# Kernel optimization log

Measured on AMD Instinct MI355X. Metric: run time of the kernel, lower is better.

## Reference

```python
import jax, jax.numpy as jnp
import numpy as np

GH, GW = 7, 7            # hierarchical grid size
LN_EPS = 1e-5            # torch nn.LayerNorm default eps
NEG = -1e9


def _adaptive_avg_pool2d(x, oh, ow):
    # Replicates torch F.adaptive_avg_pool2d bin boundaries:
    # start=floor(i*H/out), end=ceil((i+1)*H/out). x: (..., H, W)
    H, W = x.shape[-2], x.shape[-1]
    def b(i, n, o):
        return int(np.floor(i * n / o)), int(np.ceil((i + 1) * n / o))
    rows = jnp.stack([x[..., b(i, H, oh)[0]:b(i, H, oh)[1], :].mean(axis=-2)
                      for i in range(oh)], axis=-2)
    out = jnp.stack([rows[..., b(j, W, ow)[0]:b(j, W, ow)[1]].mean(axis=-1)
                     for j in range(ow)], axis=-1)
    return out


def _layernorm(y, gamma, beta):
    mu = y.mean(axis=-1, keepdims=True)
    var = jnp.mean(jnp.square(y - mu), axis=-1, keepdims=True)
    return (y - mu) * jax.lax.rsqrt(var + LN_EPS) * gamma + beta


def setup_inputs() -> dict:
    key = jax.random.key(0)
    ks = jax.random.split(key, 16)
    B, C, H, W = 8, 512, 32, 32
    heads = 8
    s = 0.02
    f32 = jnp.float32
    return {
        "x":    jax.random.normal(ks[0], (B, C, H, W), f32),
        "Wq":   jax.random.normal(ks[1], (C, C), f32) * s,
        "bq":   jnp.zeros((C,), f32),
        "Wk":   jax.random.normal(ks[2], (C, C), f32) * s,
        "bk":   jnp.zeros((C,), f32),
        "Wv":   jax.random.normal(ks[3], (C, C), f32) * s,
        "bv":   jnp.zeros((C,), f32),
        "Wo":   jax.random.normal(ks[4], (C, C), f32) * s,
        "bo":   jnp.zeros((C,), f32),
        "Wsp":  jax.random.normal(ks[5], (heads, C), f32) * s,   # 1x1 conv C->heads
        "bsp":  jnp.zeros((heads,), f32),
        "Wse1": jax.random.normal(ks[6], (C // 16, C), f32) * s, # SE squeeze
        "bse1": jnp.zeros((C // 16,), f32),
        "Wse2": jax.random.normal(ks[7], (C, C // 16), f32) * s, # SE excite
        "bse2": jnp.zeros((C,), f32),
        "gamma": jnp.ones((C,), f32),
        "beta":  jnp.zeros((C,), f32),
    }


def reference(x, Wq, bq, Wk, bk, Wv, bv, Wo, bo, Wsp, bsp,
              Wse1, bse1, Wse2, bse2, gamma, beta):
    B, C, H, W = x.shape
    heads = Wsp.shape[0]
    d = C // heads
    N = H * W

    # --- hierarchical grid mask ---
    sp = jnp.einsum('bchw,nc->bnhw', x, Wsp) + bsp[None, :, None, None]
    m = jax.nn.sigmoid(sp)                               # (B, heads, H, W)
    mg = _adaptive_avg_pool2d(m, GH, GW)
    mg = (mg > 0.5).astype(x.dtype)                      # binarize
    ih = np.floor(np.arange(H) * GH / H).astype(np.int32)  # torch 'nearest'
    iw = np.floor(np.arange(W) * GW / W).astype(np.int32)
    mask = mg[..., ih[:, None], iw[None, :]]             # (B, heads, H, W)

    # --- SE channel gating ---
    pooled = x.mean(axis=(2, 3))                         # (B, C)
    h1 = jax.nn.relu(pooled @ Wse1.T + bse1)
    cw = jax.nn.sigmoid(h1 @ Wse2.T + bse2)              # (B, C)
    xf = (x * cw[:, :, None, None]).reshape(B, C, N).transpose(0, 2, 1)  # (B,N,C)

    # --- multi-head attention with outer-product additive mask ---
    def heads_split(t):
        return t.reshape(B, N, heads, d).transpose(0, 2, 1, 3)  # (B,h,N,d)
    Q = heads_split(xf @ Wq.T + bq)
    K = heads_split(xf @ Wk.T + bk)
    V = heads_split(xf @ Wv.T + bv)

    scores = jnp.einsum('bhnd,bhmd->bhnm', Q, K) / (d ** 0.5)
    mf = mask.reshape(B, heads, N)
    bias = (1.0 - mf[:, :, :, None] * mf[:, :, None, :]) * NEG
    w = jax.nn.softmax(scores + bias, axis=-1)
    attn = jnp.einsum('bhnm,bhmd->bhnd', w, V)
    attn = attn.transpose(0, 2, 1, 3).reshape(B, N, C)
    attn = attn @ Wo.T + bo

    y = _layernorm(xf + attn, gamma, beta)               # (B, N, C)
    return y.transpose(0, 2, 1).reshape(B, C, H, W)
```

## Files before the change

### kernel.cpp

```cpp
#include <hip/hip_runtime.h>
#include <hip/hip_bf16.h>
#include <math.h>

typedef unsigned short u16;
typedef unsigned int u32;
typedef __attribute__((ext_vector_type(4))) float f32x4;
typedef __attribute__((ext_vector_type(8))) short bf16x8;
typedef __attribute__((ext_vector_type(4))) unsigned short us4;
typedef __attribute__((ext_vector_type(8))) unsigned short us8;

#define DI __device__ __forceinline__

DI u16 f2b(float x){ __hip_bfloat16 h = __float2bfloat16(x); return *reinterpret_cast<u16*>(&h); }
DI float b2f(u16 u){ union { float f; u32 i; } v; v.i = ((u32)u) << 16; return v.f; }

__global__ void k_cvt(const float* __restrict__ Wq, const float* __restrict__ Wk,
                      const float* __restrict__ Wv, const float* __restrict__ Wo,
                      u16* __restrict__ WB, u16* __restrict__ WoB){
  int i = blockIdx.x * 256 + threadIdx.x;
  WB[i]          = f2b(Wq[i]);
  WB[262144 + i] = f2b(Wk[i]);
  WB[524288 + i] = f2b(Wv[i]);
  WoB[i]         = f2b(Wo[i]);
}

__global__ __launch_bounds__(256) void k_pooled(const float* __restrict__ x, float* __restrict__ pooled){
  int row  = blockIdx.x * 4 + (threadIdx.x >> 6);
  int lane = threadIdx.x & 63;
  const float4* p = (const float4*)(x + ((size_t)row << 10));
  float4 v0 = p[lane], v1 = p[lane + 64], v2 = p[lane + 128], v3 = p[lane + 192];
  float s = (v0.x + v0.y + v0.z + v0.w) + (v1.x + v1.y + v1.z + v1.w)
          + (v2.x + v2.y + v2.z + v2.w) + (v3.x + v3.y + v3.z + v3.w);
  #pragma unroll
  for (int o = 32; o > 0; o >>= 1) s += __shfl_down(s, o, 64);
  if (lane == 0) pooled[row] = s * (1.0f / 1024.0f);
}

__global__ __launch_bounds__(256) void k_se(const float* __restrict__ pooled,
    const float* __restrict__ Wse1, const float* __restrict__ bse1,
    const float* __restrict__ Wse2, const float* __restrict__ bse2,
    float* __restrict__ cw){
  __shared__ float pl[512];
  __shared__ float h1[32];
  int b = blockIdx.x, t = threadIdx.x;
  pl[t] = pooled[b * 512 + t];
  pl[t + 256] = pooled[b * 512 + t + 256];
  __syncthreads();
  if (t < 32){
    float acc = bse1[t];
    const float* w = Wse1 + t * 512;
    for (int c = 0; c < 512; c++) acc = fmaf(pl[c], w[c], acc);
    h1[t] = fmaxf(acc, 0.0f);
  }
  __syncthreads();
  for (int c = t; c < 512; c += 256){
    float acc = bse2[c];
    const float* w = Wse2 + c * 32;
    #pragma unroll
    for (int j = 0; j < 32; j++) acc = fmaf(h1[j], w[j], acc);
    cw[b * 512 + c] = 1.0f / (1.0f + expf(-acc));
  }
}

__global__ __launch_bounds__(256) void k_sp(const float* __restrict__ x,
    const float* __restrict__ Wsp, const float* __restrict__ bsp, float* __restrict__ mbuf){
  __shared__ float wsh[4096];
  __shared__ float part[4][512];
  int t = threadIdx.x;
  for (int i = t; i < 4096; i += 256) wsh[i] = Wsp[i];
  __syncthreads();
  int b = blockIdx.x >> 4, n0 = (blockIdx.x & 15) << 6;
  int px = t & 63, cq = t >> 6;
  const float* xp = x + ((size_t)b << 19) + ((size_t)(cq * 128) << 10) + n0 + px;
  float acc[8] = {0,0,0,0,0,0,0,0};
  for (int c = 0; c < 128; c++){
    float xv = xp[(size_t)c << 10];
    #pragma unroll
    for (int h = 0; h < 8; h++) acc[h] = fmaf(xv, wsh[(h << 9) + cq * 128 + c], acc[h]);
  }
  #pragma unroll
  for (int h = 0; h < 8; h++) part[cq][(h << 6) + px] = acc[h];
  __syncthreads();
  for (int i = t; i < 512; i += 256){
    int h = i >> 6, p = i & 63;
    float s = part[0][i] + part[1][i] + part[2][i] + part[3][i] + bsp[h];
    mbuf[(((size_t)(b * 8 + h)) << 10) + n0 + p] = 1.0f / (1.0f + expf(-s));
  }
}

__global__ void k_mask(const float* __restrict__ mbuf, float* __restrict__ bneg){
  __shared__ float sm[1024];
  __shared__ float mg[49];
  int bh = blockIdx.x, t = threadIdx.x;
  const float* mp = mbuf + ((size_t)bh << 10);
  for (int i = t; i < 1024; i += 64) sm[i] = mp[i];
  __syncthreads();
  if (t < 49){
    int ci = t / 7, cj = t % 7;
    int r0 = (ci * 32) / 7, r1 = ((ci + 1) * 32 + 6) / 7;
    int c0 = (cj * 32) / 7, c1 = ((cj + 1) * 32 + 6) / 7;
    float acc = 0.0f;
    for (int cc = c0; cc < c1; cc++){
      float rs = 0.0f;
      for (int rr = r0; rr < r1; rr++) rs += sm[rr * 32 + cc];
      acc += rs / (float)(r1 - r0);
    }
    float v = acc / (float)(c1 - c0);
    mg[t] = (v > 0.5f) ? 1.0f : 0.0f;
  }
  __syncthreads();
  for (int i = t; i < 1024; i += 64){
    int r = i >> 5, c = i & 31;
    float m = mg[((r * 7) >> 5) * 7 + ((c * 7) >> 5)];
    bneg[((size_t)bh << 10) + i] = (m > 0.5f) ? 0.0f : -1e9f;
  }
}

__global__ __launch_bounds__(256) void k_xf(const float* __restrict__ x,
    const float* __restrict__ cw, u16* __restrict__ xfB){
  __shared__ float tile[64][65];
  int bid = blockIdx.x;
  int b = bid >> 7, c0 = ((bid >> 4) & 7) << 6, n0 = (bid & 15) << 6;
  int t = threadIdx.x;
  {
    int cl = t >> 2, nc = (t & 3) << 4;
    const float* xp = x + ((size_t)(b * 512 + c0 + cl) << 10) + n0 + nc;
    float cwv = cw[b * 512 + c0 + cl];
    #pragma unroll
    for (int i = 0; i < 16; i += 4){
      float4 v = *(const float4*)(xp + i);
      tile[cl][nc + i + 0] = v.x * cwv;
      tile[cl][nc + i + 1] = v.y * cwv;
      tile[cl][nc + i + 2] = v.z * cwv;
      tile[cl][nc + i + 3] = v.w * cwv;
    }
  }
  __syncthreads();
  {
    int nl = t >> 2, cc = (t & 3) << 4;
    u16* op = xfB + ((size_t)(b * 1024 + n0 + nl) << 9) + c0 + cc;
    us8 o0, o1;
    #pragma unroll
    for (int i = 0; i < 8; i++)  o0[i] = f2b(tile[cc + i][nl]);
    #pragma unroll
    for (int i = 0; i < 8; i++)  o1[i] = f2b(tile[cc + 8 + i][nl]);
    *(us8*)op = o0;
    *(us8*)(op + 8) = o1;
  }
}

template<int MODE>
__global__ __launch_bounds__(256) void k_gemm(const u16* __restrict__ A, const u16* __restrict__ Bw,
    const float* __restrict__ b0, const float* __restrict__ b1, const float* __restrict__ b2,
    u16* __restrict__ outQ, u16* __restrict__ outK, u16* __restrict__ outV, float* __restrict__ outF){
  __shared__ u16 As[128 * 40];
  __shared__ u16 Bs[128 * 40];
  int m0 = blockIdx.x * 128, n0 = blockIdx.y * 128;
  int t = threadIdx.x, lane = t & 63, w = t >> 6;
  int wr = w >> 1, wc = w & 1;
  f32x4 acc[4][4];
  #pragma unroll
  for (int mt = 0; mt < 4; mt++)
    #pragma unroll
    for (int nt = 0; nt < 4; nt++) acc[mt][nt] = (f32x4){0.f, 0.f, 0.f, 0.f};

  int srow = t >> 1, scol = (t & 1) << 4;
  const u16* ap = A  + (size_t)(m0 + srow) * 512 + scol;
  const u16* bp = Bw + (size_t)(n0 + srow) * 512 + scol;

  for (int k0 = 0; k0 < 512; k0 += 32){
    uint4 av0 = *(const uint4*)(ap + k0);
    uint4 av1 = *(const uint4*)(ap + k0 + 8);
    uint4 bv0 = *(const uint4*)(bp + k0);
    uint4 bv1 = *(const uint4*)(bp + k0 + 8);
    *(uint4*)&As[srow * 40 + scol]     = av0;
    *(uint4*)&As[srow * 40 + scol + 8] = av1;
    *(uint4*)&Bs[srow * 40 + scol]     = bv0;
    *(uint4*)&Bs[srow * 40 + scol + 8] = bv1;
    __syncthreads();
    bf16x8 afr[4], bfr[4];
    #pragma unroll
    for (int mt = 0; mt < 4; mt++)
      afr[mt] = *(bf16x8*)&As[(wr * 64 + mt * 16 + (lane & 15)) * 40 + ((lane >> 4) << 3)];
    #pragma unroll
    for (int nt = 0; nt < 4; nt++)
      bfr[nt] = *(bf16x8*)&Bs[(wc * 64 + nt * 16 + (lane & 15)) * 40 + ((lane >> 4) << 3)];
    #pragma unroll
    for (int mt = 0; mt < 4; mt++)
      #pragma unroll
      for (int nt = 0; nt < 4; nt++)
        acc[mt][nt] = __builtin_amdgcn_mfma_f32_16x16x32_bf16(afr[mt], bfr[nt], acc[mt][nt], 0, 0, 0);
    __syncthreads();
  }

  #pragma unroll
  for (int mt = 0; mt < 4; mt++){
    #pragma unroll
    for (int nt = 0; nt < 4; nt++){
      int o = n0 + wc * 64 + nt * 16 + (lane & 15);
      int mb = m0 + wr * 64 + mt * 16 + ((lane >> 4) << 2);
      if (MODE == 0){
        int which = o >> 9, c = o & 511;
        int h = c >> 6, d = c & 63;
        int b = mb >> 10, n = mb & 1023;
        if (which == 2){
          float bias = b2[c];
          int nperm = (n & ~31) + (((n >> 2) & 3) << 3) + (((n >> 4) & 1) << 2);
          us4 pk;
          #pragma unroll
          for (int j = 0; j < 4; j++) pk[j] = f2b(acc[mt][nt][j] + bias);
          *(us4*)&outV[(((size_t)(b * 8 + h)) << 16) + ((size_t)d << 10) + nperm] = pk;
        } else {
          float bias = (which == 0) ? b0[c] : b1[c];
          u16* base = (which == 0) ? outQ : outK;
          #pragma unroll
          for (int j = 0; j < 4; j++)
            base[(((size_t)(b * 8 + h)) << 16) + ((size_t)(n + j) << 6) + d] = f2b(acc[mt][nt][j] + bias);
        }
      } else {
        float bias = b0[o];
        #pragma unroll
        for (int j = 0; j < 4; j++)
          outF[((size_t)(mb + j) << 9) + o] = acc[mt][nt][j] + bias;
      }
    }
  }
}

__global__ __launch_bounds__(256) void k_flash(const u16* __restrict__ Q, const u16* __restrict__ K,
    const u16* __restrict__ Vt, const float* __restrict__ bneg, u16* __restrict__ attnB){
  __shared__ u16 Ks[64 * 72];
  __shared__ u16 Vts[64 * 72];
  __shared__ float mks[64];
  int bid = blockIdx.x;
  int bh = bid >> 4, q0 = (bid & 15) << 6;
  int t = threadIdx.x, lane = t & 63, w = t >> 6;
  int g = lane >> 4, li = lane & 15;

  const u16* Kp = K  + ((size_t)bh << 16);
  const u16* Vp = Vt + ((size_t)bh << 16);
  const float* bp = bneg + ((size_t)bh << 10);

  bf16x8 qfr0, qfr1;
  {
    const u16* qrow = Q + ((size_t)bh << 16) + ((size_t)(q0 + w * 16 + li) << 6);
    qfr0 = *(const bf16x8*)(qrow + g * 8);
    qfr1 = *(const bf16x8*)(qrow + 32 + g * 8);
  }
  float bnq = bp[q0 + w * 16 + li];

  f32x4 oacc[4];
  #pragma unroll
  for (int dt = 0; dt < 4; dt++) oacc[dt] = (f32x4){0.f, 0.f, 0.f, 0.f};
  float mrun = -INFINITY, lrun = 0.0f;

  int sr = t >> 2, sc = (t & 3) << 4;
  const u16* kg = Kp + ((size_t)sr << 6) + sc;
  const u16* vg = Vp + ((size_t)sr << 10) + sc;
  uint4 kr0, kr1, vr0, vr1;
  float mr = 0.0f;
  kr0 = *(const uint4*)(kg);
  kr1 = *(const uint4*)(kg + 8);
  vr0 = *(const uint4*)(vg);
  vr1 = *(const uint4*)(vg + 8);
  if (t < 64) mr = bp[t];

  for (int kt = 0; kt < 16; kt++){
    __syncthreads();
    *(uint4*)&Ks[sr * 72 + sc]      = kr0;
    *(uint4*)&Ks[sr * 72 + sc + 8]  = kr1;
    *(uint4*)&Vts[sr * 72 + sc]     = vr0;
    *(uint4*)&Vts[sr * 72 + sc + 8] = vr1;
    if (t < 64) mks[t] = mr;
    if (kt < 15){
      kr0 = *(const uint4*)(kg + (kt + 1) * 4096);
      kr1 = *(const uint4*)(kg + (kt + 1) * 4096 + 8);
      vr0 = *(const uint4*)(vg + (kt + 1) * 64);
      vr1 = *(const uint4*)(vg + (kt + 1) * 64 + 8);
      if (t < 64) mr = bp[(kt + 1) * 64 + t];
    }
    __syncthreads();

    f32x4 sacc[4];
    #pragma unroll
    for (int mt = 0; mt < 4; mt++) sacc[mt] = (f32x4){0.f, 0.f, 0.f, 0.f};
    #pragma unroll
    for (int mt = 0; mt < 4; mt++){
      bf16x8 kfr0 = *(bf16x8*)&Ks[(mt * 16 + li) * 72 + g * 8];
      bf16x8 kfr1 = *(bf16x8*)&Ks[(mt * 16 + li) * 72 + 32 + g * 8];
      sacc[mt] = __builtin_amdgcn_mfma_f32_16x16x32_bf16(kfr0, qfr0, sacc[mt], 0, 0, 0);
      sacc[mt] = __builtin_amdgcn_mfma_f32_16x16x32_bf16(kfr1, qfr1, sacc[mt], 0, 0, 0);
    }

    float tmax = -INFINITY;
    #pragma unroll
    for (int mt = 0; mt < 4; mt++){
      float4 bk = *(const float4*)&mks[mt * 16 + g * 4];
      float bkk[4] = {bk.x, bk.y, bk.z, bk.w};
      #pragma unroll
      for (int j = 0; j < 4; j++){
        float s = sacc[mt][j] * 0.125f + fminf(bkk[j], bnq);
        sacc[mt][j] = s;
        tmax = fmaxf(tmax, s);
      }
    }
    tmax = fmaxf(tmax, __shfl_xor(tmax, 16, 64));
    tmax = fmaxf(tmax, __shfl_xor(tmax, 32, 64));
    float mnew = fmaxf(mrun, tmax);
    float scl = __expf(mrun - mnew);
    mrun = mnew;

    float rsum = 0.0f;
    #pragma unroll
    for (int mt = 0; mt < 4; mt++)
      #pragma unroll
      for (int j = 0; j < 4; j++){
        float p = __expf(sacc[mt][j] - mnew);
        sacc[mt][j] = p;
        rsum += p;
      }
    rsum += __shfl_xor(rsum, 16, 64);
    rsum += __shfl_xor(rsum, 32, 64);
    lrun = lrun * scl + rsum;
    #pragma unroll
    for (int dt = 0; dt < 4; dt++)
      #pragma unroll
      for (int j = 0; j < 4; j++) oacc[dt][j] *= scl;

    bf16x8 pfr0, pfr1;
    #pragma unroll
    for (int e = 0; e < 4; e++){
      pfr0[e]     = (short)f2b(sacc[0][e]);
      pfr0[4 + e] = (short)f2b(sacc[1][e]);
      pfr1[e]     = (short)f2b(sacc[2][e]);
      pfr1[4 + e] = (short)f2b(sacc[3][e]);
    }
    #pragma unroll
    for (int dt = 0; dt < 4; dt++){
      bf16x8 vfr0 = *(bf16x8*)&Vts[(dt * 16 + li) * 72 + g * 8];
      bf16x8 vfr1 = *(bf16x8*)&Vts[(dt * 16 + li) * 72 + 32 + g * 8];
      oacc[dt] = __builtin_amdgcn_mfma_f32_16x16x32_bf16(vfr0, pfr0, oacc[dt], 0, 0, 0);
      oacc[dt] = __builtin_amdgcn_mfma_f32_16x16x32_bf16(vfr1, pfr1, oacc[dt], 0, 0, 0);
    }
  }

  float inv = 1.0f / lrun;
  int b = bh >> 3, h = bh & 7;
  u16* op = attnB + (((size_t)(b * 1024 + q0 + w * 16 + li)) << 9) + h * 64 + g * 4;
  #pragma unroll
  for (int dt = 0; dt < 4; dt++){
    us4 pk;
    #pragma unroll
    for (int j = 0; j < 4; j++) pk[j] = f2b(oacc[dt][j] * inv);
    *(us4*)(op + dt * 16) = pk;
  }
}

__global__ __launch_bounds__(256) void k_ln(const u16* __restrict__ xfB, const float* __restrict__ attnO,
    const float* __restrict__ gamma, const float* __restrict__ beta, float* __restrict__ out){
  __shared__ float mu_s[64], rs_s[64];
  __shared__ float tile[64][65];
  int b = blockIdx.x >> 4, n0 = (blockIdx.x & 15) << 6;
  int t = threadIdx.x, w = t >> 6, lane = t & 63;

  for (int r = w * 16; r < w * 16 + 16; r++){
    size_t rb = ((size_t)(b * 1024 + n0 + r)) << 9;
    const float* ap = attnO + rb + lane * 8;
    const u16*  xp = xfB + rb + lane * 8;
    float4 a0 = *(const float4*)ap;
    float4 a1 = *(const float4*)(ap + 4);
    union { uint4 v; u16 u[8]; } xv; xv.v = *(const uint4*)xp;
    float v0 = a0.x + b2f(xv.u[0]), v1 = a0.y + b2f(xv.u[1]);
    float v2 = a0.z + b2f(xv.u[2]), v3 = a0.w + b2f(xv.u[3]);
    float v4 = a1.x + b2f(xv.u[4]), v5 = a1.y + b2f(xv.u[5]);
    float v6 = a1.z + b2f(xv.u[6]), v7 = a1.w + b2f(xv.u[7]);
    float s  = v0 + v1 + v2 + v3 + v4 + v5 + v6 + v7;
    float s2 = v0*v0 + v1*v1 + v2*v2 + v3*v3 + v4*v4 + v5*v5 + v6*v6 + v7*v7;
    #pragma unroll
    for (int o = 32; o > 0; o >>= 1){ s += __shfl_xor(s, o, 64); s2 += __shfl_xor(s2, o, 64); }
    if (lane == 0){
      float mu = s * (1.0f / 512.0f);
      float var = s2 * (1.0f / 512.0f) - mu * mu;
      mu_s[r] = mu;
      rs_s[r] = 1.0f / sqrtf(var + 1e-5f);
    }
  }
  __syncthreads();

  for (int ch = 0; ch < 8; ch++){
    int c0 = ch * 64;
    {
      int r = t >> 2, cp = (t & 3) << 4;
      size_t rb = (((size_t)(b * 1024 + n0 + r)) << 9) + c0 + cp;
      float mu = mu_s[r], rstd = rs_s[r];
      #pragma unroll
      for (int i2 = 0; i2 < 2; i2++){
        float4 a0 = *(const float4*)(attnO + rb + i2 * 8);
        float4 a1 = *(const float4*)(attnO + rb + i2 * 8 + 4);
        union { uint4 v; u16 u[8]; } xv; xv.v = *(const uint4*)(xfB + rb + i2 * 8);
        float vv[8] = { a0.x + b2f(xv.u[0]), a0.y + b2f(xv.u[1]), a0.z + b2f(xv.u[2]), a0.w + b2f(xv.u[3]),
                        a1.x + b2f(xv.u[4]), a1.y + b2f(xv.u[5]), a1.z + b2f(xv.u[6]), a1.w + b2f(xv.u[7]) };
        #pragma unroll
        for (int i = 0; i < 8; i++){
          int c = c0 + cp + i2 * 8 + i;
          tile[r][cp + i2 * 8 + i] = (vv[i] - mu) * rstd * gamma[c] + beta[c];
        }
      }
    }
    __syncthreads();
    {
      int cl = t >> 2, np_ = (t & 3) << 4;
      float* op = out + (((size_t)(b * 512 + c0 + cl)) << 10) + n0 + np_;
      #pragma unroll
      for (int i = 0; i < 16; i += 4){
        float4 vo = { tile[np_ + i][cl], tile[np_ + i + 1][cl], tile[np_ + i + 2][cl], tile[np_ + i + 3][cl] };
        *(float4*)(op + i) = vo;
      }
    }
    __syncthreads();
  }
}

extern "C" void kernel_launch(void* const* d_in, const int* in_sizes, int n_in,
                              void* d_out, int out_size, void* d_ws, size_t ws_size,
                              hipStream_t stream){
  (void)in_sizes; (void)n_in; (void)out_size; (void)ws_size;
  const float* x    = (const float*)d_in[0];
  const float* Wq   = (const float*)d_in[1];
  const float* bq   = (const float*)d_in[2];
  const float* Wk   = (const float*)d_in[3];
  const float* bk   = (const float*)d_in[4];
  const float* Wv   = (const float*)d_in[5];
  const float* bv   = (const float*)d_in[6];
  const float* Wo   = (const float*)d_in[7];
  const float* bo   = (const float*)d_in[8];
  const float* Wsp  = (const float*)d_in[9];
  const float* bsp  = (const float*)d_in[10];
  const float* Wse1 = (const float*)d_in[11];
  const float* bse1 = (const float*)d_in[12];
  const float* Wse2 = (const float*)d_in[13];
  const float* bse2 = (const float*)d_in[14];
  const float* gamma= (const float*)d_in[15];
  const float* beta = (const float*)d_in[16];
  float* out = (float*)d_out;

  char* ws = (char*)d_ws;
  size_t off = 0;
  auto alloc = [&](size_t bytes) -> void* {
    void* p = ws + off;
    off += (bytes + 255) & ~(size_t)255;
    return p;
  };
  u16*   WB     = (u16*)  alloc(1536 * 512 * 2);
  u16*   WoB    = (u16*)  alloc(512 * 512 * 2);
  float* pooled = (float*)alloc(4096 * 4);
  float* cw     = (float*)alloc(4096 * 4);
  float* mbuf   = (float*)alloc(65536 * 4);
  float* bneg   = (float*)alloc(65536 * 4);
  u16*   xfB    = (u16*)  alloc((size_t)8192 * 512 * 2);
  u16*   Qb     = (u16*)  alloc(8388608);
  u16*   Kb     = (u16*)  alloc(8388608);
  u16*   VtG    = (u16*)  alloc(8388608);
  u16*   attnB  = (u16*)  alloc(8388608);
  float* attnO  = (float*)Qb;

  k_cvt   <<<dim3(1024), dim3(256), 0, stream>>>(Wq, Wk, Wv, Wo, WB, WoB);
  k_pooled<<<dim3(1024), dim3(256), 0, stream>>>(x, pooled);
  k_se    <<<dim3(8),    dim3(256), 0, stream>>>(pooled, Wse1, bse1, Wse2, bse2, cw);
  k_sp    <<<dim3(128),  dim3(256), 0, stream>>>(x, Wsp, bsp, mbuf);
  k_mask  <<<dim3(64),   dim3(64),  0, stream>>>(mbuf, bneg);
  k_xf    <<<dim3(1024), dim3(256), 0, stream>>>(x, cw, xfB);
  k_gemm<0><<<dim3(64, 12), dim3(256), 0, stream>>>(xfB, WB, bq, bk, bv, Qb, Kb, VtG, (float*)nullptr);
  k_flash <<<dim3(1024), dim3(256), 0, stream>>>(Qb, Kb, VtG, bneg, attnB);
  k_gemm<1><<<dim3(64, 4), dim3(256), 0, stream>>>(attnB, WoB, bo, bo, bo, nullptr, nullptr, nullptr, attnO);
  k_ln    <<<dim3(128),  dim3(256), 0, stream>>>(xfB, attnO, gamma, beta, out);
}
```

Baseline: 156.5 us.

## Pipeline GEMM with K=64 register prefetch, split-KV flash with lazy rescale

New measurement: 209.6 us (median of 3 runs). +34.0%, slower.

```diff
diff --git a/kernel.cpp b/kernel.cpp
--- a/kernel.cpp
+++ b/kernel.cpp
@@ -153,43 +153,64 @@
 __global__ __launch_bounds__(256) void k_gemm(const u16* __restrict__ A, const u16* __restrict__ Bw,
     const float* __restrict__ b0, const float* __restrict__ b1, const float* __restrict__ b2,
     u16* __restrict__ outQ, u16* __restrict__ outK, u16* __restrict__ outV, float* __restrict__ outF){
-  __shared__ u16 As[128 * 40];
-  __shared__ u16 Bs[128 * 40];
+  __shared__ __align__(16) u16 As[128 * 72];
+  __shared__ __align__(16) u16 Bs[128 * 72];
   int m0 = blockIdx.x * 128, n0 = blockIdx.y * 128;
+  bool vblk = (MODE == 0) && (n0 >= 1024);
   int t = threadIdx.x, lane = t & 63, w = t >> 6;
   int wr = w >> 1, wc = w & 1;
+  int g = lane >> 4, li = lane & 15;
   f32x4 acc[4][4];
   #pragma unroll
   for (int mt = 0; mt < 4; mt++)
     #pragma unroll
     for (int nt = 0; nt < 4; nt++) acc[mt][nt] = (f32x4){0.f, 0.f, 0.f, 0.f};
 
-  int srow = t >> 1, scol = (t & 1) << 4;
+  int srow = t >> 1, scol = (t & 1) << 5;
   const u16* ap = A  + (size_t)(m0 + srow) * 512 + scol;
   const u16* bp = Bw + (size_t)(n0 + srow) * 512 + scol;
 
-  for (int k0 = 0; k0 < 512; k0 += 32){
-    uint4 av0 = *(const uint4*)(ap + k0);
-    uint4 av1 = *(const uint4*)(ap + k0 + 8);
-    uint4 bv0 = *(const uint4*)(bp + k0);
-    uint4 bv1 = *(const uint4*)(bp + k0 + 8);
-    *(uint4*)&As[srow * 40 + scol]     = av0;
-    *(uint4*)&As[srow * 40 + scol + 8] = av1;
-    *(uint4*)&Bs[srow * 40 + scol]     = bv0;
-    *(uint4*)&Bs[srow * 40 + scol + 8] = bv1;
+  uint4 pa[4], pb[4];
+  #pragma unroll
+  for (int j = 0; j < 4; j++){ pa[j] = *(const uint4*)(ap + j * 8); pb[j] = *(const uint4*)(bp + j * 8); }
+
+  for (int k0 = 0; k0 < 512; k0 += 64){
+    #pragma unroll
+    for (int j = 0; j < 4; j++){
+      *(uint4*)&As[srow * 72 + scol + j * 8] = pa[j];
+      *(uint4*)&Bs[srow * 72 + scol + j * 8] = pb[j];
+    }
     __syncthreads();
-    bf16x8 afr[4], bfr[4];
-    #pragma unroll
-    for (int mt = 0; mt < 4; mt++)
-      afr[mt] = *(bf16x8*)&As[(wr * 64 + mt * 16 + (lane & 15)) * 40 + ((lane >> 4) << 3)];
-    #pragma unroll
-    for (int nt = 0; nt < 4; nt++)
-      bfr[nt] = *(bf16x8*)&Bs[(wc * 64 + nt * 16 + (lane & 15)) * 40 + ((lane >> 4) << 3)];
-    #pragma unroll
-    for (int mt = 0; mt < 4; mt++)
+    if (k0 < 448){
+      #pragma unroll
+      for (int j = 0; j < 4; j++){
+        pa[j] = *(const uint4*)(ap + k0 + 64 + j * 8);
+        pb[j] = *(const uint4*)(bp + k0 + 64 + j * 8);
+      }
+    }
+    #pragma unroll
+    for (int kk = 0; kk < 2; kk++){
+      bf16x8 afr[4], bfr[4];
+      #pragma unroll
+      for (int mt = 0; mt < 4; mt++)
+        afr[mt] = *(bf16x8*)&As[(wr * 64 + mt * 16 + li) * 72 + kk * 32 + g * 8];
       #pragma unroll
       for (int nt = 0; nt < 4; nt++)
-        acc[mt][nt] = __builtin_amdgcn_mfma_f32_16x16x32_bf16(afr[mt], bfr[nt], acc[mt][nt], 0, 0, 0);
+        bfr[nt] = *(bf16x8*)&Bs[(wc * 64 + nt * 16 + li) * 72 + kk * 32 + g * 8];
+      if (vblk){
+        #pragma unroll
+        for (int mt = 0; mt < 4; mt++)
+          #pragma unroll
+          for (int nt = 0; nt < 4; nt++)
+            acc[mt][nt] = __builtin_amdgcn_mfma_f32_16x16x32_bf16(afr[mt], bfr[nt], acc[mt][nt], 0, 0, 0);
+      } else {
+        #pragma unroll
+        for (int mt = 0; mt < 4; mt++)
+          #pragma unroll
+          for (int nt = 0; nt < 4; nt++)
+            acc[mt][nt] = __builtin_amdgcn_mfma_f32_16x16x32_bf16(bfr[nt], afr[mt], acc[mt][nt], 0, 0, 0);
+      }
+    }
     __syncthreads();
   }
 
@@ -197,44 +218,54 @@
   for (int mt = 0; mt < 4; mt++){
     #pragma unroll
     for (int nt = 0; nt < 4; nt++){
-      int o = n0 + wc * 64 + nt * 16 + (lane & 15);
-      int mb = m0 + wr * 64 + mt * 16 + ((lane >> 4) << 2);
-      if (MODE == 0){
-        int which = o >> 9, c = o & 511;
-        int h = c >> 6, d = c & 63;
+      if (MODE == 0 && vblk){
+        int o = n0 + wc * 64 + nt * 16 + li;
+        int c = o & 511, h = c >> 6, d = c & 63;
+        int mb = m0 + wr * 64 + mt * 16 + (g << 2);
         int b = mb >> 10, n = mb & 1023;
-        if (which == 2){
-          float bias = b2[c];
-          int nperm = (n & ~31) + (((n >> 2) & 3) << 3) + (((n >> 4) & 1) << 2);
-          us4 pk;
-          #pragma unroll
-          for (int j = 0; j < 4; j++) pk[j] = f2b(acc[mt][nt][j] + bias);
-          *(us4*)&outV[(((size_t)(b * 8 + h)) << 16) + ((size_t)d << 10) + nperm] = pk;
-        } else {
-          float bias = (which == 0) ? b0[c] : b1[c];
-          u16* base = (which == 0) ? outQ : outK;
-          #pragma unroll
-          for (int j = 0; j < 4; j++)
-            base[(((size_t)(b * 8 + h)) << 16) + ((size_t)(n + j) << 6) + d] = f2b(acc[mt][nt][j] + bias);
-        }
+        float bias = b2[c];
+        int nperm = (n & ~31) + (((n >> 2) & 3) << 3) + (((n >> 4) & 1) << 2);
+        us4 pk;
+        #pragma unroll
+        for (int j = 0; j < 4; j++) pk[j] = f2b(acc[mt][nt][j] + bias);
+        *(us4*)&outV[(((size_t)(b * 8 + h)) << 16) + ((size_t)d << 10) + nperm] = pk;
+      } else if (MODE == 0){
+        int m = m0 + wr * 64 + mt * 16 + li;
+        int b = m >> 10, n = m & 1023;
+        int obase = n0 + wc * 64 + nt * 16;
+        int which = obase >> 9;
+        int c = obase & 511, h = c >> 6;
+        int dloc = (c & 63) + (g << 2);
+        const float* bb = which ? b1 : b0;
+        float4 bias4 = *(const float4*)&bb[c + (g << 2)];
+        float bk4[4] = {bias4.x, bias4.y, bias4.z, bias4.w};
+        u16* base = which ? outK : outQ;
+        us4 pk;
+        #pragma unroll
+        for (int j = 0; j < 4; j++) pk[j] = f2b(acc[mt][nt][j] + bk4[j]);
+        *(us4*)&base[(((size_t)(b * 8 + h)) << 16) + ((size_t)n << 6) + dloc] = pk;
       } else {
-        float bias = b0[o];
-        #pragma unroll
-        for (int j = 0; j < 4; j++)
-          outF[((size_t)(mb + j) << 9) + o] = acc[mt][nt][j] + bias;
-      }
-    }
-  }
-}
-
-__global__ __launch_bounds__(256) void k_flash(const u16* __restrict__ Q, const u16* __restrict__ K,
+        int m = m0 + wr * 64 + mt * 16 + li;
+        int obase = n0 + wc * 64 + nt * 16 + (g << 2);
+        float4 bias4 = *(const float4*)&b0[obase];
+        float4 vo = { acc[mt][nt][0] + bias4.x, acc[mt][nt][1] + bias4.y,
+                      acc[mt][nt][2] + bias4.z, acc[mt][nt][3] + bias4.w };
+        *(float4*)&outF[(size_t)m * 512 + obase] = vo;
+      }
+    }
+  }
+}
+
+__global__ __launch_bounds__(512) void k_flash(const u16* __restrict__ Q, const u16* __restrict__ K,
     const u16* __restrict__ Vt, const float* __restrict__ bneg, u16* __restrict__ attnB){
-  __shared__ u16 Ks[64 * 72];
-  __shared__ u16 Vts[64 * 72];
-  __shared__ float mks[64];
-  int bid = blockIdx.x;
+  __shared__ __align__(16) u16 Ks[2][64 * 72];
+  __shared__ __align__(16) u16 Vts[2][64 * 72];
+  __shared__ float mks[2][64];
+  int hw = blockIdx.x;
+  int bid = ((hw & 7) << 7) + (hw >> 3);
   int bh = bid >> 4, q0 = (bid & 15) << 6;
   int t = threadIdx.x, lane = t & 63, w = t >> 6;
+  int qw = w & 3, half = w >> 2;
   int g = lane >> 4, li = lane & 15;
 
   const u16* Kp = K  + ((size_t)bh << 16);
@@ -243,41 +274,39 @@
 
   bf16x8 qfr0, qfr1;
   {
-    const u16* qrow = Q + ((size_t)bh << 16) + ((size_t)(q0 + w * 16 + li) << 6);
+    const u16* qrow = Q + ((size_t)bh << 16) + ((size_t)(q0 + qw * 16 + li) << 6);
     qfr0 = *(const bf16x8*)(qrow + g * 8);
     qfr1 = *(const bf16x8*)(qrow + 32 + g * 8);
   }
-  float bnq = bp[q0 + w * 16 + li];
+  float bnq = bp[q0 + qw * 16 + li];
 
   f32x4 oacc[4];
   #pragma unroll
   for (int dt = 0; dt < 4; dt++) oacc[dt] = (f32x4){0.f, 0.f, 0.f, 0.f};
   float mrun = -INFINITY, lrun = 0.0f;
 
-  int sr = t >> 2, sc = (t & 3) << 4;
-  const u16* kg = Kp + ((size_t)sr << 6) + sc;
-  const u16* vg = Vp + ((size_t)sr << 10) + sc;
-  uint4 kr0, kr1, vr0, vr1;
-  float mr = 0.0f;
-  kr0 = *(const uint4*)(kg);
-  kr1 = *(const uint4*)(kg + 8);
-  vr0 = *(const uint4*)(vg);
-  vr1 = *(const uint4*)(vg + 8);
-  if (t < 64) mr = bp[t];
-
-  for (int kt = 0; kt < 16; kt++){
+  int tl = t & 255, sset = t >> 8;
+  int sr = tl >> 2, sc = (tl & 3) << 4;
+  const u16* kg = Kp + (sr << 6) + sc + (sset << 12);
+  const u16* vg = Vp + (sr << 10) + sc + (sset << 6);
+  uint4 kr0 = *(const uint4*)kg,       kr1 = *(const uint4*)(kg + 8);
+  uint4 vr0 = *(const uint4*)vg,       vr1 = *(const uint4*)(vg + 8);
+  float mr = (tl < 64) ? bp[(sset << 6) + tl] : 0.0f;
+
+  for (int i = 0; i < 8; i++){
     __syncthreads();
-    *(uint4*)&Ks[sr * 72 + sc]      = kr0;
-    *(uint4*)&Ks[sr * 72 + sc + 8]  = kr1;
-    *(uint4*)&Vts[sr * 72 + sc]     = vr0;
-    *(uint4*)&Vts[sr * 72 + sc + 8] = vr1;
-    if (t < 64) mks[t] = mr;
-    if (kt < 15){
-      kr0 = *(const uint4*)(kg + (kt + 1) * 4096);
-      kr1 = *(const uint4*)(kg + (kt + 1) * 4096 + 8);
-      vr0 = *(const uint4*)(vg + (kt + 1) * 64);
-      vr1 = *(const uint4*)(vg + (kt + 1) * 64 + 8);
-      if (t < 64) mr = bp[(kt + 1) * 64 + t];
+    *(uint4*)&Ks[sset][sr * 72 + sc]      = kr0;
+    *(uint4*)&Ks[sset][sr * 72 + sc + 8]  = kr1;
+    *(uint4*)&Vts[sset][sr * 72 + sc]     = vr0;
+    *(uint4*)&Vts[sset][sr * 72 + sc + 8] = vr1;
+    if (tl < 64) mks[sset][tl] = mr;
+    if (i < 7){
+      int off = (i + 1) << 1;
+      kr0 = *(const uint4*)(kg + off * 4096);
+      kr1 = *(const uint4*)(kg + off * 4096 + 8);
+      vr0 = *(const uint4*)(vg + off * 64);
+      vr1 = *(const uint4*)(vg + off * 64 + 8);
+      if (tl < 64) mr = bp[((off + sset) << 6) + tl];
     }
     __syncthreads();
 
@@ -286,8 +315,8 @@
     for (int mt = 0; mt < 4; mt++) sacc[mt] = (f32x4){0.f, 0.f, 0.f, 0.f};
     #pragma unroll
     for (int mt = 0; mt < 4; mt++){
-      bf16x8 kfr0 = *(bf16x8*)&Ks[(mt * 16 + li) * 72 + g * 8];
-      bf16x8 kfr1 = *(bf16x8*)&Ks[(mt * 16 + li) * 72 + 32 + g * 8];
+      bf16x8 kfr0 = *(bf16x8*)&Ks[half][(mt * 16 + li) * 72 + g * 8];
+      bf16x8 kfr1 = *(bf16x8*)&Ks[half][(mt * 16 + li) * 72 + 32 + g * 8];
       sacc[mt] = __builtin_amdgcn_mfma_f32_16x16x32_bf16(kfr0, qfr0, sacc[mt], 0, 0, 0);
       sacc[mt] = __builtin_amdgcn_mfma_f32_16x16x32_bf16(kfr1, qfr1, sacc[mt], 0, 0, 0);
     }
@@ -295,7 +324,7 @@
     float tmax = -INFINITY;
     #pragma unroll
     for (int mt = 0; mt < 4; mt++){
-      float4 bk = *(const float4*)&mks[mt * 16 + g * 4];
+      float4 bk = *(const float4*)&mks[half][mt * 16 + g * 4];
       float bkk[4] = {bk.x, bk.y, bk.z, bk.w};
       #pragma unroll
       for (int j = 0; j < 4; j++){
@@ -306,26 +335,30 @@
     }
     tmax = fmaxf(tmax, __shfl_xor(tmax, 16, 64));
     tmax = fmaxf(tmax, __shfl_xor(tmax, 32, 64));
-    float mnew = fmaxf(mrun, tmax);
-    float scl = __expf(mrun - mnew);
-    mrun = mnew;
+
+    if (!__all(tmax <= mrun + 8.0f)){
+      float mnew = fmaxf(mrun, tmax);
+      float scl = __expf(mrun - mnew);
+      mrun = mnew;
+      lrun *= scl;
+      #pragma unroll
+      for (int dt = 0; dt < 4; dt++)
+        #pragma unroll
+        for (int j = 0; j < 4; j++) oacc[dt][j] *= scl;
+    }
 
     float rsum = 0.0f;
     #pragma unroll
     for (int mt = 0; mt < 4; mt++)
       #pragma unroll
       for (int j = 0; j < 4; j++){
-        float p = __expf(sacc[mt][j] - mnew);
+        float p = __expf(sacc[mt][j] - mrun);
         sacc[mt][j] = p;
         rsum += p;
       }
     rsum += __shfl_xor(rsum, 16, 64);
     rsum += __shfl_xor(rsum, 32, 64);
-    lrun = lrun * scl + rsum;
-    #pragma unroll
-    for (int dt = 0; dt < 4; dt++)
-      #pragma unroll
-      for (int j = 0; j < 4; j++) oacc[dt][j] *= scl;
+    lrun += rsum;
 
     bf16x8 pfr0, pfr1;
     #pragma unroll
@@ -337,22 +370,40 @@
     }
     #pragma unroll
     for (int dt = 0; dt < 4; dt++){
-      bf16x8 vfr0 = *(bf16x8*)&Vts[(dt * 16 + li) * 72 + g * 8];
-      bf16x8 vfr1 = *(bf16x8*)&Vts[(dt * 16 + li) * 72 + 32 + g * 8];
+      bf16x8 vfr0 = *(bf16x8*)&Vts[half][(dt * 16 + li) * 72 + g * 8];
+      bf16x8 vfr1 = *(bf16x8*)&Vts[half][(dt * 16 + li) * 72 + 32 + g * 8];
       oacc[dt] = __builtin_amdgcn_mfma_f32_16x16x32_bf16(vfr0, pfr0, oacc[dt], 0, 0, 0);
       oacc[dt] = __builtin_amdgcn_mfma_f32_16x16x32_bf16(vfr1, pfr1, oacc[dt], 0, 0, 0);
     }
   }
 
-  float inv = 1.0f / lrun;
-  int b = bh >> 3, h = bh & 7;
-  u16* op = attnB + (((size_t)(b * 1024 + q0 + w * 16 + li)) << 9) + h * 64 + g * 4;
-  #pragma unroll
-  for (int dt = 0; dt < 4; dt++){
-    us4 pk;
-    #pragma unroll
-    for (int j = 0; j < 4; j++) pk[j] = f2b(oacc[dt][j] * inv);
-    *(us4*)(op + dt * 16) = pk;
+  __syncthreads();
+  float* pm = (float*)&Ks[0][0];
+  float* pl = pm + 256;
+  float* po = pl + 256;
+  int slot = qw * 64 + lane;
+  if (half == 1){
+    pm[slot] = mrun;
+    pl[slot] = lrun;
+    #pragma unroll
+    for (int dt = 0; dt < 4; dt++) *(f32x4*)&po[slot * 16 + dt * 4] = oacc[dt];
+  }
+  __syncthreads();
+  if (half == 0){
+    float mb = pm[slot], lb = pl[slot];
+    float mm = fmaxf(mrun, mb);
+    float ea = __expf(mrun - mm), eb = __expf(mb - mm);
+    float linv = 1.0f / (lrun * ea + lb * eb);
+    int b = bh >> 3, h = bh & 7;
+    u16* op = attnB + (((size_t)(b * 1024 + q0 + qw * 16 + li)) << 9) + h * 64 + g * 4;
+    #pragma unroll
+    for (int dt = 0; dt < 4; dt++){
+      f32x4 ob = *(f32x4*)&po[slot * 16 + dt * 4];
+      us4 pk;
+      #pragma unroll
+      for (int j = 0; j < 4; j++) pk[j] = f2b((oacc[dt][j] * ea + ob[j] * eb) * linv);
+      *(us4*)(op + dt * 16) = pk;
+    }
   }
 }
 
@@ -471,7 +522,7 @@
   k_mask  <<<dim3(64),   dim3(64),  0, stream>>>(mbuf, bneg);
   k_xf    <<<dim3(1024), dim3(256), 0, stream>>>(x, cw, xfB);
   k_gemm<0><<<dim3(64, 12), dim3(256), 0, stream>>>(xfB, WB, bq, bk, bv, Qb, Kb, VtG, (float*)nullptr);
-  k_flash <<<dim3(1024), dim3(256), 0, stream>>>(Qb, Kb, VtG, bneg, attnB);
+  k_flash <<<dim3(1024), dim3(512), 0, stream>>>(Qb, Kb, VtG, bneg, attnB);
   k_gemm<1><<<dim3(64, 4), dim3(256), 0, stream>>>(attnB, WoB, bo, bo, bo, nullptr, nullptr, nullptr, attnO);
   k_ln    <<<dim3(128),  dim3(256), 0, stream>>>(xfB, attnO, gamma, beta, out);
 }
```

## Rework QKV GEMM pipeline and epilogue; lazy softmax rescale and block swizzle in flash

Applied to the files above, without the earlier changes.

Measured after the change: 207.7 us. 1.33x slower.

```diff
diff --git a/kernel.cpp b/kernel.cpp
--- a/kernel.cpp
+++ b/kernel.cpp
@@ -153,86 +153,148 @@
 __global__ __launch_bounds__(256) void k_gemm(const u16* __restrict__ A, const u16* __restrict__ Bw,
     const float* __restrict__ b0, const float* __restrict__ b1, const float* __restrict__ b2,
     u16* __restrict__ outQ, u16* __restrict__ outK, u16* __restrict__ outV, float* __restrict__ outF){
-  __shared__ u16 As[128 * 40];
-  __shared__ u16 Bs[128 * 40];
+  __shared__ __align__(16) u16 smem[18432];
+  u16* As = smem;
+  u16* Bs = smem + 9216;
   int m0 = blockIdx.x * 128, n0 = blockIdx.y * 128;
+  bool vblk = (MODE == 0) && (n0 >= 1024);
   int t = threadIdx.x, lane = t & 63, w = t >> 6;
   int wr = w >> 1, wc = w & 1;
+  int g = lane >> 4, li = lane & 15;
   f32x4 acc[4][4];
   #pragma unroll
   for (int mt = 0; mt < 4; mt++)
     #pragma unroll
     for (int nt = 0; nt < 4; nt++) acc[mt][nt] = (f32x4){0.f, 0.f, 0.f, 0.f};
 
-  int srow = t >> 1, scol = (t & 1) << 4;
+  int srow = t >> 1, scol = (t & 1) << 5;
   const u16* ap = A  + (size_t)(m0 + srow) * 512 + scol;
   const u16* bp = Bw + (size_t)(n0 + srow) * 512 + scol;
 
-  for (int k0 = 0; k0 < 512; k0 += 32){
-    uint4 av0 = *(const uint4*)(ap + k0);
-    uint4 av1 = *(const uint4*)(ap + k0 + 8);
-    uint4 bv0 = *(const uint4*)(bp + k0);
-    uint4 bv1 = *(const uint4*)(bp + k0 + 8);
-    *(uint4*)&As[srow * 40 + scol]     = av0;
-    *(uint4*)&As[srow * 40 + scol + 8] = av1;
-    *(uint4*)&Bs[srow * 40 + scol]     = bv0;
-    *(uint4*)&Bs[srow * 40 + scol + 8] = bv1;
+  uint4 pa[4], pb[4];
+  #pragma unroll
+  for (int j = 0; j < 4; j++){ pa[j] = *(const uint4*)(ap + j * 8); pb[j] = *(const uint4*)(bp + j * 8); }
+
+  for (int k0 = 0; k0 < 512; k0 += 64){
+    #pragma unroll
+    for (int j = 0; j < 4; j++){
+      *(uint4*)&As[srow * 72 + scol + j * 8] = pa[j];
+      *(uint4*)&Bs[srow * 72 + scol + j * 8] = pb[j];
+    }
     __syncthreads();
-    bf16x8 afr[4], bfr[4];
-    #pragma unroll
-    for (int mt = 0; mt < 4; mt++)
-      afr[mt] = *(bf16x8*)&As[(wr * 64 + mt * 16 + (lane & 15)) * 40 + ((lane >> 4) << 3)];
-    #pragma unroll
-    for (int nt = 0; nt < 4; nt++)
-      bfr[nt] = *(bf16x8*)&Bs[(wc * 64 + nt * 16 + (lane & 15)) * 40 + ((lane >> 4) << 3)];
-    #pragma unroll
-    for (int mt = 0; mt < 4; mt++)
+    if (k0 < 448){
+      #pragma unroll
+      for (int j = 0; j < 4; j++){
+        pa[j] = *(const uint4*)(ap + k0 + 64 + j * 8);
+        pb[j] = *(const uint4*)(bp + k0 + 64 + j * 8);
+      }
+    }
+    #pragma unroll
+    for (int kk = 0; kk < 2; kk++){
+      bf16x8 afr[4], bfr[4];
+      #pragma unroll
+      for (int mt = 0; mt < 4; mt++)
+        afr[mt] = *(bf16x8*)&As[(wr * 64 + mt * 16 + li) * 72 + kk * 32 + g * 8];
       #pragma unroll
       for (int nt = 0; nt < 4; nt++)
-        acc[mt][nt] = __builtin_amdgcn_mfma_f32_16x16x32_bf16(afr[mt], bfr[nt], acc[mt][nt], 0, 0, 0);
+        bfr[nt] = *(bf16x8*)&Bs[(wc * 64 + nt * 16 + li) * 72 + kk * 32 + g * 8];
+      if (vblk){
+        #pragma unroll
+        for (int mt = 0; mt < 4; mt++)
+          #pragma unroll
+          for (int nt = 0; nt < 4; nt++)
+            acc[mt][nt] = __builtin_amdgcn_mfma_f32_16x16x32_bf16(afr[mt], bfr[nt], acc[mt][nt], 0, 0, 0);
+      } else {
+        #pragma unroll
+        for (int mt = 0; mt < 4; mt++)
+          #pragma unroll
+          for (int nt = 0; nt < 4; nt++)
+            acc[mt][nt] = __builtin_amdgcn_mfma_f32_16x16x32_bf16(bfr[nt], afr[mt], acc[mt][nt], 0, 0, 0);
+      }
+    }
     __syncthreads();
   }
 
-  #pragma unroll
-  for (int mt = 0; mt < 4; mt++){
-    #pragma unroll
-    for (int nt = 0; nt < 4; nt++){
-      int o = n0 + wc * 64 + nt * 16 + (lane & 15);
-      int mb = m0 + wr * 64 + mt * 16 + ((lane >> 4) << 2);
-      if (MODE == 0){
-        int which = o >> 9, c = o & 511;
-        int h = c >> 6, d = c & 63;
-        int b = mb >> 10, n = mb & 1023;
-        if (which == 2){
-          float bias = b2[c];
-          int nperm = (n & ~31) + (((n >> 2) & 3) << 3) + (((n >> 4) & 1) << 2);
-          us4 pk;
-          #pragma unroll
-          for (int j = 0; j < 4; j++) pk[j] = f2b(acc[mt][nt][j] + bias);
-          *(us4*)&outV[(((size_t)(b * 8 + h)) << 16) + ((size_t)d << 10) + nperm] = pk;
-        } else {
-          float bias = (which == 0) ? b0[c] : b1[c];
-          u16* base = (which == 0) ? outQ : outK;
-          #pragma unroll
-          for (int j = 0; j < 4; j++)
-            base[(((size_t)(b * 8 + h)) << 16) + ((size_t)(n + j) << 6) + d] = f2b(acc[mt][nt][j] + bias);
-        }
-      } else {
-        float bias = b0[o];
+  if (MODE == 1){
+    #pragma unroll
+    for (int mt = 0; mt < 4; mt++){
+      #pragma unroll
+      for (int nt = 0; nt < 4; nt++){
+        int m = m0 + wr * 64 + mt * 16 + li;
+        int obase = n0 + wc * 64 + nt * 16 + (g << 2);
+        float4 bias4 = *(const float4*)&b0[obase];
+        float4 vo = { acc[mt][nt][0] + bias4.x, acc[mt][nt][1] + bias4.y,
+                      acc[mt][nt][2] + bias4.z, acc[mt][nt][3] + bias4.w };
+        *(float4*)&outF[(size_t)m * 512 + obase] = vo;
+      }
+    }
+    return;
+  }
+
+  u16* Cl = smem;
+  if (vblk){
+    #pragma unroll
+    for (int mt = 0; mt < 4; mt++){
+      #pragma unroll
+      for (int nt = 0; nt < 4; nt++){
+        int ol = wc * 64 + nt * 16 + li;
+        float bias = b2[(n0 & 511) + ol];
+        int mperm = wr * 64 + ((mt >> 1) << 5) + (g << 3) + ((mt & 1) << 2);
+        us4 pk;
         #pragma unroll
-        for (int j = 0; j < 4; j++)
-          outF[((size_t)(mb + j) << 9) + o] = acc[mt][nt][j] + bias;
-      }
+        for (int j = 0; j < 4; j++) pk[j] = f2b(acc[mt][nt][j] + bias);
+        *(us4*)&Cl[ol * 136 + mperm] = pk;
+      }
+    }
+  } else {
+    const float* bb = (n0 >> 9) ? b1 : b0;
+    #pragma unroll
+    for (int mt = 0; mt < 4; mt++){
+      #pragma unroll
+      for (int nt = 0; nt < 4; nt++){
+        int ml = wr * 64 + mt * 16 + li;
+        int ob = wc * 64 + nt * 16 + (g << 2);
+        float4 bias4 = *(const float4*)&bb[(n0 & 511) + ob];
+        float bk4[4] = {bias4.x, bias4.y, bias4.z, bias4.w};
+        us4 pk;
+        #pragma unroll
+        for (int j = 0; j < 4; j++) pk[j] = f2b(acc[mt][nt][j] + bk4[j]);
+        *(us4*)&Cl[ml * 136 + ob] = pk;
+      }
+    }
+  }
+  __syncthreads();
+
+  if (vblk){
+    int b = m0 >> 10, nt0 = m0 & 1023;
+    #pragma unroll
+    for (int p = 0; p < 8; p++){
+      int r = p * 16 + (t >> 4);
+      int c = (n0 & 511) + r, h = c >> 6, dv = c & 63;
+      us8 v = *(us8*)&Cl[r * 136 + ((t & 15) << 3)];
+      *(us8*)&outV[(((size_t)(b * 8 + h)) << 16) + ((size_t)dv << 10) + nt0 + ((t & 15) << 3)] = v;
+    }
+  } else {
+    u16* base = (n0 >> 9) ? outK : outQ;
+    #pragma unroll
+    for (int p = 0; p < 8; p++){
+      int r = p * 16 + (t >> 4);
+      int m = m0 + r, b = m >> 10, n = m & 1023;
+      int ol = (t & 15) << 3;
+      int c = (n0 & 511) + ol, h = c >> 6, dv = c & 63;
+      us8 v = *(us8*)&Cl[r * 136 + ol];
+      *(us8*)&base[(((size_t)(b * 8 + h)) << 16) + ((size_t)n << 6) + dv] = v;
     }
   }
 }
 
 __global__ __launch_bounds__(256) void k_flash(const u16* __restrict__ Q, const u16* __restrict__ K,
     const u16* __restrict__ Vt, const float* __restrict__ bneg, u16* __restrict__ attnB){
-  __shared__ u16 Ks[64 * 72];
-  __shared__ u16 Vts[64 * 72];
+  __shared__ __align__(16) u16 Ks[64 * 72];
+  __shared__ __align__(16) u16 Vts[64 * 72];
   __shared__ float mks[64];
-  int bid = blockIdx.x;
+  int hw = blockIdx.x;
+  int bid = ((hw & 7) << 7) + (hw >> 3);
   int bh = bid >> 4, q0 = (bid & 15) << 6;
   int t = threadIdx.x, lane = t & 63, w = t >> 6;
   int g = lane >> 4, li = lane & 15;
@@ -306,26 +368,30 @@
     }
     tmax = fmaxf(tmax, __shfl_xor(tmax, 16, 64));
     tmax = fmaxf(tmax, __shfl_xor(tmax, 32, 64));
-    float mnew = fmaxf(mrun, tmax);
-    float scl = __expf(mrun - mnew);
-    mrun = mnew;
+
+    if (!__all(tmax <= mrun + 8.0f)){
+      float mnew = fmaxf(mrun, tmax);
+      float scl = __expf(mrun - mnew);
+      mrun = mnew;
+      lrun *= scl;
+      #pragma unroll
+      for (int dt = 0; dt < 4; dt++)
+        #pragma unroll
+        for (int j = 0; j < 4; j++) oacc[dt][j] *= scl;
+    }
 
     float rsum = 0.0f;
     #pragma unroll
     for (int mt = 0; mt < 4; mt++)
       #pragma unroll
       for (int j = 0; j < 4; j++){
-        float p = __expf(sacc[mt][j] - mnew);
+        float p = __expf(sacc[mt][j] - mrun);
         sacc[mt][j] = p;
         rsum += p;
       }
     rsum += __shfl_xor(rsum, 16, 64);
     rsum += __shfl_xor(rsum, 32, 64);
-    lrun = lrun * scl + rsum;
-    #pragma unroll
-    for (int dt = 0; dt < 4; dt++)
-      #pragma unroll
-      for (int j = 0; j < 4; j++) oacc[dt][j] *= scl;
+    lrun += rsum;
 
     bf16x8 pfr0, pfr1;
     #pragma unroll
```
